# Kernel optimization log

Hardware: AMD Instinct MI355X
Metric: run time of the kernel (lower is better)

## Reference

```python
import jax, jax.numpy as jnp
import numpy as np
import math

B, S, D, H = 8, 256, 4096, 16
HD = D // H  # 256 == S, so the module's transposed mask application is exactly elementwise


def setup_inputs() -> dict:
    key = jax.random.key(0)
    ks = jax.random.split(key, 12)
    sc = 1.0 / math.sqrt(D)
    inp = {
        "q": jax.random.normal(ks[0], (B, S, D), dtype=jnp.float32),
        "k": jax.random.normal(ks[1], (B, S, D), dtype=jnp.float32),
        "v": jax.random.normal(ks[2], (B, S, D), dtype=jnp.float32),
        "mask": jax.random.randint(ks[3], (B, S), 0, 2),
        "Wq": jax.random.normal(ks[4], (D, D), dtype=jnp.float32) * sc,
        "bq": jnp.zeros((D,), dtype=jnp.float32),
        "Wk": jax.random.normal(ks[5], (D, D), dtype=jnp.float32) * sc,
        "bk": jnp.zeros((D,), dtype=jnp.float32),
        "Wv": jax.random.normal(ks[6], (D, D), dtype=jnp.float32) * sc,
        "bv": jnp.zeros((D,), dtype=jnp.float32),
        "Wo": jax.random.normal(ks[7], (D, D), dtype=jnp.float32) * sc,
        "bo": jnp.zeros((D,), dtype=jnp.float32),
    }
    return inp


def reference(q, k, v, mask, Wq, bq, Wk, bk, Wv, bv, Wo, bo):
    def proj(x, W, b):
        # nn.Linear: x @ W.T + b ; then [B,S,H,HD] -> [B,H,S,HD]
        return (x @ W.T + b).reshape(B, S, H, HD).transpose(0, 2, 1, 3)

    qh = proj(q, Wq, bq)
    kh = proj(k, Wk, bk)
    vh = proj(v, Wv, bv)

    # torch: attn_mask = (mask==0).view(bs,1,1,-1).repeat(1,H,HD,1) -> [B,H,HD,S]
    # then where(attn_mask, 0, q) against q of shape [B,H,S,HD] (elementwise since HD==S)
    am = jnp.broadcast_to((mask == 0)[:, None, None, :], (B, H, HD, S))
    qh = jnp.where(am, 0.0, qh)
    kh = jnp.where(am, 0.0, kh)

    scale = 1.0 / math.sqrt(HD)
    scores = jnp.einsum('bhqd,bhkd->bhqk', qh, kh) * scale
    w = jax.nn.softmax(scores, axis=-1)
    out = jnp.einsum('bhqk,bhkd->bhqd', w, vh)
    out = out.transpose(0, 2, 1, 3).reshape(B, S, D)
    out = out * (D ** -0.5)
    return out @ Wo.T + bo
```

## Files before the change

### kernel.cpp

```cpp
#include <hip/hip_runtime.h>


typedef _Float16 f16;
typedef f16 f16x8 __attribute__((ext_vector_type(8)));
typedef float f32x4 __attribute__((ext_vector_type(4)));

__device__ __forceinline__ void g2lds(const f16* g, f16* l) {
  __builtin_amdgcn_global_load_lds((const __attribute__((address_space(1))) void*)g,
                                   (__attribute__((address_space(3))) void*)l, 16, 0, 0);
}

__device__ __forceinline__ void cvt8(const float* src, f16* dst, int i) {
  float4 a = *(const float4*)(src + i);
  float4 b = *(const float4*)(src + i + 4);
  f16x8 o;
  o[0] = (f16)a.x; o[1] = (f16)a.y; o[2] = (f16)a.z; o[3] = (f16)a.w;
  o[4] = (f16)b.x; o[5] = (f16)b.y; o[6] = (f16)b.z; o[7] = (f16)b.w;
  *(f16x8*)(dst + i) = o;
}

__global__ __launch_bounds__(256) void cvt_x(const float* __restrict__ q,
                                             const float* __restrict__ k,
                                             const float* __restrict__ v,
                                             f16* __restrict__ oq, f16* __restrict__ ok,
                                             f16* __restrict__ ov) {
  const float* src; f16* dst;
  if (blockIdx.y == 0)      { src = q; dst = oq; }
  else if (blockIdx.y == 1) { src = k; dst = ok; }
  else                      { src = v; dst = ov; }
  cvt8(src, dst, (blockIdx.x * 256 + threadIdx.x) * 8);
}

__global__ __launch_bounds__(256) void cvt_w2(const float* __restrict__ a,
                                              const float* __restrict__ b,
                                              f16* __restrict__ oa, f16* __restrict__ ob) {
  const float* src; f16* dst;
  if (blockIdx.y == 0) { src = a; dst = oa; }
  else                 { src = b; dst = ob; }
  cvt8(src, dst, (blockIdx.x * 256 + threadIdx.x) * 8);
}

#define MFMA8x(ACC, FA, FB, MO, NO)                                             \
  do {                                                                          \
    __builtin_amdgcn_s_setprio(1);                                              \
    _Pragma("unroll")                                                           \
    for (int m_ = 0; m_ < (MO); ++m_)                                           \
      _Pragma("unroll")                                                         \
      for (int n_ = 0; n_ < (NO); ++n_)                                         \
        _Pragma("unroll")                                                       \
        for (int ks_ = 0; ks_ < 2; ++ks_)                                       \
          ACC = __builtin_amdgcn_mfma_f32_16x16x32_f16(FA[m_][ks_], FB[n_][ks_],\
                                                       ACC, 0, 0, 0);           \
    __builtin_amdgcn_s_setprio(0);                                              \
  } while (0)

__global__ __launch_bounds__(512, 2) void gemm256(
    const f16* __restrict__ Aq, const f16* __restrict__ Ak,
    const float* __restrict__ Bq, const float* __restrict__ Bk,
    const float* __restrict__ bq, const float* __restrict__ bk,
    const int* __restrict__ mask,
    f16* __restrict__ Qbh, f16* __restrict__ Kbh)
{
  __shared__ __align__(16) f16 lds[2][4][8192];
  const int tid = threadIdx.x;
  const int lane = tid & 63, wid = tid >> 6;
  const int wm = wid >> 2, wn = wid & 3;
  const int ln = lane & 15, lh = lane >> 4;
  const int lnx = ln & 7;
  const int K = 4096, NT = 64;

  const int seg = blockIdx.x >> 7;
  int inner = blockIdx.x & 127;
  inner = (inner & 7) * 16 + (inner >> 3);

  const f16* A     = (seg == 0) ? Aq : Ak;
  const float* B   = (seg == 0) ? Bq : Bk;
  const float* bias = (seg == 0) ? bq : bk;
  const int bm = inner % 8, bn = inner / 8;

  const size_t Abase = (size_t)bm * 256 * K;
  const size_t Bbase = (size_t)bn * 256 * K;

  const int sr = tid >> 3;
  const int ss = (tid & 7) ^ (sr & 7);
  const int br = tid >> 2;
  const int bj = tid & 3;
  const int bs0 = ((bj * 2) ^ (br & 7)) * 8;
  const int bs1 = ((bj * 2 + 1) ^ (br & 7)) * 8;

#define STAGE_A(tt, bb_)                                                         \
  do {                                                                           \
    const int kt_ = (tt) << 6;                                                   \
    g2lds(A + Abase + (size_t)sr * K + kt_ + ss * 8,        &lds[bb_][0][0] + tid * 8); \
    g2lds(A + Abase + (size_t)(64 + sr) * K + kt_ + ss * 8, &lds[bb_][0][0] + (512 + tid) * 8); \
    g2lds(A + Abase + (size_t)(128 + sr) * K + kt_ + ss * 8, &lds[bb_][1][0] + tid * 8); \
    g2lds(A + Abase + (size_t)(192 + sr) * K + kt_ + ss * 8, &lds[bb_][1][0] + (512 + tid) * 8); \
  } while (0)

  float4 rb0, rb1, rb2, rb3, rb4, rb5, rb6, rb7;

#define BLOAD(tt)                                                                \
  do {                                                                           \
    const int kt_ = (tt) << 6;                                                   \
    const float* p0_ = B + Bbase + (size_t)br * K + kt_ + bj * 16;               \
    const float* p1_ = B + Bbase + (size_t)(128 + br) * K + kt_ + bj * 16;       \
    rb0 = *(const float4*)(p0_);      rb1 = *(const float4*)(p0_ + 4);           \
    rb2 = *(const float4*)(p0_ + 8);  rb3 = *(const float4*)(p0_ + 12);          \
    rb4 = *(const float4*)(p1_);      rb5 = *(const float4*)(p1_ + 4);           \
    rb6 = *(const float4*)(p1_ + 8);  rb7 = *(const float4*)(p1_ + 12);          \
  } while (0)

#define PACK8(w_, xa_, xb_)                                                      \
  do {                                                                           \
    w_[0] = (f16)xa_.x; w_[1] = (f16)xa_.y; w_[2] = (f16)xa_.z; w_[3] = (f16)xa_.w; \
    w_[4] = (f16)xb_.x; w_[5] = (f16)xb_.y; w_[6] = (f16)xb_.z; w_[7] = (f16)xb_.w; \
  } while (0)

#define BWRITE(bb_)                                                              \
  do {                                                                           \
    f16x8 w0_, w1_, w2_, w3_;                                                    \
    PACK8(w0_, rb0, rb1); PACK8(w1_, rb2, rb3);                                  \
    PACK8(w2_, rb4, rb5); PACK8(w3_, rb6, rb7);                                  \
    *(f16x8*)(&lds[bb_][2][0] + br * 64 + bs0) = w0_;                            \
    *(f16x8*)(&lds[bb_][2][0] + br * 64 + bs1) = w1_;                            \
    *(f16x8*)(&lds[bb_][3][0] + br * 64 + bs0) = w2_;                            \
    *(f16x8*)(&lds[bb_][3][0] + br * 64 + bs1) = w3_;                            \
  } while (0)

#define RD_A03(buf) do { _Pragma("unroll")                                       \
  for (int m_ = 0; m_ < 4; ++m_) _Pragma("unroll")                               \
    for (int k_ = 0; k_ < 2; ++k_)                                               \
      a03[m_][k_] = *(const f16x8*)&(buf)[(m_ * 16 + ln) * 64 + ((k_ * 4 + lh) ^ lnx) * 8]; } while (0)
#define RD_A47(buf) do { _Pragma("unroll")                                       \
  for (int m_ = 0; m_ < 4; ++m_) _Pragma("unroll")                               \
    for (int k_ = 0; k_ < 2; ++k_)                                               \
      a47[m_][k_] = *(const f16x8*)&(buf)[((64 + m_ * 16) + ln) * 64 + ((k_ * 4 + lh) ^ lnx) * 8]; } while (0)
#define RD_B01(buf) do { _Pragma("unroll")                                       \
  for (int n_ = 0; n_ < 2; ++n_) _Pragma("unroll")                               \
    for (int k_ = 0; k_ < 2; ++k_)                                               \
      b01[n_][k_] = *(const f16x8*)&(buf)[(brow + n_ * 16 + ln) * 64 + ((k_ * 4 + lh) ^ lnx) * 8]; } while (0)
#define RD_B23(buf) do { _Pragma("unroll")                                       \
  for (int n_ = 0; n_ < 2; ++n_) _Pragma("unroll")                               \
    for (int k_ = 0; k_ < 2; ++k_)                                               \
      b23[n_][k_] = *(const f16x8*)&(buf)[(brow + 32 + n_ * 16 + ln) * 64 + ((k_ * 4 + lh) ^ lnx) * 8]; } while (0)

  f32x4 acc[8][4] = {};
  f16x8 a03[4][2], a47[4][2], b01[2][2], b23[2][2];
  const int brow = (wn & 1) * 64;

  STAGE_A(0, 0); BLOAD(0);
  asm volatile("s_waitcnt vmcnt(0)" ::: "memory");
  BWRITE(0);
  asm volatile("s_waitcnt lgkmcnt(0)" ::: "memory");
  __builtin_amdgcn_s_barrier();
  {
    const f16* cA0 = &lds[0][wm][0];
    const f16* cB0 = &lds[0][2 + (wn >> 1)][0];
    RD_A03(cA0); RD_B01(cB0);
  }

  for (int t = 0; t < NT; ++t) {
    const int bb = t & 1;
    const f16* cA = &lds[bb][wm][0];
    const f16* cAn = &lds[bb ^ 1][wm][0];
    const f16* cB = &lds[bb][2 + (wn >> 1)][0];
    const f16* cBn = &lds[bb ^ 1][2 + (wn >> 1)][0];

    if (t + 1 < NT) { STAGE_A(t + 1, bb ^ 1); BLOAD(t + 1); }
    RD_B23(cB);
    __builtin_amdgcn_s_barrier();
    MFMA8x(acc[m_][n_], a03, b01, 4, 2);

    RD_A47(cA);
    __builtin_amdgcn_s_barrier();
    MFMA8x(acc[m_][2 + n_], a03, b23, 4, 2);

    __builtin_amdgcn_s_barrier();
    MFMA8x(acc[4 + m_][n_], a47, b01, 4, 2);

    if (t + 1 < NT) {
      asm volatile("s_waitcnt vmcnt(0)" ::: "memory");
      BWRITE(bb ^ 1);
    }
    asm volatile("s_waitcnt lgkmcnt(0)" ::: "memory");
    __builtin_amdgcn_s_barrier();
    if (t + 1 < NT) { RD_A03(cAn); RD_B01(cBn); }
    MFMA8x(acc[4 + m_][2 + n_], a47, b23, 4, 2);
  }
#undef STAGE_A
#undef BLOAD
#undef PACK8
#undef BWRITE
#undef RD_A03
#undef RD_A47
#undef RD_B01
#undef RD_B23

#pragma unroll
  for (int mf = 0; mf < 8; ++mf)
#pragma unroll
    for (int nf = 0; nf < 4; ++nf)
#pragma unroll
      for (int i = 0; i < 4; ++i) {
        int R = bm * 256 + wm * 128 + mf * 16 + lh * 4 + i;
        int C = bn * 256 + wn * 64 + nf * 16 + ln;
        float v = acc[mf][nf][i];
        v += bias[C];
        v = mask[(R >> 8) * 256 + (C & 255)] ? v : 0.0f;
        f16* o = (seg == 0) ? Qbh : Kbh;
        o[(size_t)((R >> 8) * 16 + (C >> 8)) * 65536 +
          (size_t)(R & 255) * 256 + (C & 255)] = (f16)v;
      }
}

template<int EPI>
__global__ __launch_bounds__(512, 2) void gemm_dp(
    const f16* __restrict__ A, const f16* __restrict__ B,
    const float* __restrict__ bias, void* __restrict__ out,
    int M, int N, int K)
{
  __shared__ __align__(16) f16 lds[3 * 24576];
  const int tid = threadIdx.x;
  const int lane = tid & 63, wid = tid >> 6;
  const int wm = wid >> 2, wn = wid & 3;
  const int ln = lane & 15, lh = lane >> 4;
  const int bm = blockIdx.y, bn = blockIdx.x;

  const size_t Abase = (size_t)bm * 128 * K;
  const size_t Bbase = (size_t)bn * 256 * K;
  const int sr = tid >> 3;
  const int ss = (tid & 7) ^ (sr & 7);
  const int NT = K >> 6;

  f16* p0 = &lds[0];
  f16* p1 = &lds[24576];
  f16* p2 = &lds[2 * 24576];

#define STAGE(t_, bo_, part)                                                    \
  do {                                                                          \
    const int kt_ = (t_) << 6;                                                  \
    if ((part) == 0) {                                                          \
      g2lds(A + Abase + (size_t)sr * K + kt_ + ss * 8,         (bo_) + tid * 8);  \
      g2lds(B + Bbase + (size_t)sr * K + kt_ + ss * 8,         (bo_) + 8192 + tid * 8); \
      g2lds(B + Bbase + (size_t)(64 + sr) * K + kt_ + ss * 8,  (bo_) + 8192 + (512 + tid) * 8); \
    } else {                                                                    \
      g2lds(A + Abase + (size_t)(64 + sr) * K + kt_ + ss * 8,  (bo_) + (512 + tid) * 8); \
      g2lds(B + Bbase + (size_t)(128 + sr) * K + kt_ + ss * 8, (bo_) + 8192 + (1024 + tid) * 8); \
      g2lds(B + Bbase + (size_t)(192 + sr) * K + kt_ + ss * 8, (bo_) + 8192 + (1536 + tid) * 8); \
    }                                                                           \
  } while (0)

  const int lx = ln & 7;
  const int arow = (wm * 64 + ln) * 64;
  const int brow = (wn * 64 + ln) * 64;

#define LOADFRAGS(fa, fb, buf, ks)                                              \
  do {                                                                          \
    const f16* bA_ = (buf);                                                     \
    const f16* bB_ = (buf) + 8192;                                              \
    const int so_ = (((ks) * 4 + lh) ^ lx) * 8;                                 \
    _Pragma("unroll")                                                           \
    for (int mf = 0; mf < 4; ++mf)                                              \
      fa[mf] = *(const f16x8*)&bA_[arow + mf * 1024 + so_];                     \
    _Pragma("unroll")                                                           \
    for (int nf = 0; nf < 4; ++nf)                                              \
      fb[nf] = *(const f16x8*)&bB_[brow + nf * 1024 + so_];                     \
  } while (0)

#define MFMA16(fa, fb)                                                          \
  do {                                                                          \
    __builtin_amdgcn_s_setprio(1);                                              \
    _Pragma("unroll")                                                           \
    for (int mf = 0; mf < 4; ++mf)                                              \
      _Pragma("unroll")                                                         \
      for (int nf = 0; nf < 4; ++nf)                                            \
        acc[mf][nf] = __builtin_amdgcn_mfma_f32_16x16x32_f16(fa[mf], fb[nf],    \
                                                             acc[mf][nf], 0, 0, 0); \
    __builtin_amdgcn_s_setprio(0);                                              \
  } while (0)

  f32x4 acc[4][4] = {};
  f16x8 ca[4], cb[4], na[4], nb[4];

  STAGE(0, p0, 0); STAGE(0, p0, 1);
  STAGE(1, p1, 0); STAGE(1, p1, 1);
  asm volatile("s_waitcnt vmcnt(6)" ::: "memory");
  __builtin_amdgcn_s_barrier();
  asm volatile("" ::: "memory");
  LOADFRAGS(ca, cb, p0, 0);

  for (int t = 0; t < NT; ++t) {
    LOADFRAGS(na, nb, p0, 1);
    if (t + 2 < NT) { STAGE(t + 2, p2, 0); STAGE(t + 2, p2, 1); }
    MFMA16(ca, cb);

    if (t + 1 < NT) {
      if (t + 2 < NT) {
        asm volatile("s_waitcnt vmcnt(6)" ::: "memory");
      } else {
        asm volatile("s_waitcnt vmcnt(0)" ::: "memory");
      }
      __builtin_amdgcn_s_barrier();
      asm volatile("" ::: "memory");
      LOADFRAGS(ca, cb, p1, 0);
      MFMA16(na, nb);
      asm volatile("" ::: "memory");
      __builtin_amdgcn_s_barrier();
      asm volatile("" ::: "memory");
      f16* tp = p0; p0 = p1; p1 = p2; p2 = tp;
    } else {
      MFMA16(na, nb);
    }
  }
#undef STAGE
#undef LOADFRAGS
#undef MFMA16

#pragma unroll
  for (int mf = 0; mf < 4; ++mf)
#pragma unroll
    for (int nf = 0; nf < 4; ++nf)
#pragma unroll
      for (int i = 0; i < 4; ++i) {
        int R = bm * 128 + wm * 64 + mf * 16 + lh * 4 + i;
        int C = bn * 256 + wn * 64 + nf * 16 + ln;
        float v = acc[mf][nf][i];
        if (EPI == 1) {
          v += bias[R];
          ((f16*)out)[(size_t)(C >> 8) * 1048576 + (size_t)R * 256 + (C & 255)] = (f16)v;
        } else {
          v += bias[C];
          ((float*)out)[(size_t)R * N + C] = v;
        }
      }
}

__global__ __launch_bounds__(256) void attn_kernel(
    const f16* __restrict__ Q, const f16* __restrict__ Kt,
    const f16* __restrict__ Vt, f16* __restrict__ aout)
{
  __shared__ __align__(16) f16 tile[64 * 256];
  __shared__ __align__(16) f16 pbuf[64 * 256];
  const int tid = threadIdx.x;
  const int lane = tid & 63, w = tid >> 6;
  const int ln = lane & 15, lh = lane >> 4;
  const int bh = blockIdx.x >> 2, rb = blockIdx.x & 3;
  const int b = bh >> 4, h = bh & 15;
  const size_t hb = (size_t)bh * 65536;

  const int strow = tid >> 5;
  const int stsl  = (tid & 31) ^ (strow & 7);

  f16x8 aq[8];
  {
    const f16* qp = Q + hb + (size_t)(rb * 64 + w * 16 + ln) * 256;
#pragma unroll
    for (int ks = 0; ks < 8; ++ks)
      aq[ks] = *(const f16x8*)(qp + ks * 32 + lh * 8);
  }

  f32x4 sacc[16] = {};

  for (int kt = 0; kt < 4; ++kt) {
#pragma unroll
    for (int c = 0; c < 8; ++c) {
      int L = c * 256 + tid;
      int row = c * 8 + strow;
      g2lds(Kt + hb + (size_t)(kt * 64 + row) * 256 + stsl * 8, &tile[L * 8]);
    }
    __syncthreads();
#pragma unroll
    for (int nf = 0; nf < 4; ++nf) {
      f16x8 bf[8];
#pragma unroll
      for (int ks = 0; ks < 8; ++ks) {
        int r = nf * 16 + ln;
        int sl = (ks * 4 + lh) ^ (r & 7);
        bf[ks] = *(const f16x8*)&tile[r * 256 + sl * 8];
      }
#pragma unroll
      for (int ks = 0; ks < 8; ++ks)
        sacc[kt * 4 + nf] = __builtin_amdgcn_mfma_f32_16x16x32_f16(
            aq[ks], bf[ks], sacc[kt * 4 + nf], 0, 0, 0);
    }
    __syncthreads();
  }

  const float SC = 1.0f / 16.0f;
  float mrow[4] = {-1e30f, -1e30f, -1e30f, -1e30f};
#pragma unroll
  for (int t = 0; t < 16; ++t)
#pragma unroll
    for (int i = 0; i < 4; ++i) mrow[i] = fmaxf(mrow[i], sacc[t][i]);
#pragma unroll
  for (int i = 0; i < 4; ++i) {
    mrow[i] = fmaxf(mrow[i], __shfl_xor(mrow[i], 1));
    mrow[i] = fmaxf(mrow[i], __shfl_xor(mrow[i], 2));
    mrow[i] = fmaxf(mrow[i], __shfl_xor(mrow[i], 4));
    mrow[i] = fmaxf(mrow[i], __shfl_xor(mrow[i], 8));
  }
  float ssum[4] = {0.f, 0.f, 0.f, 0.f};
#pragma unroll
  for (int t = 0; t < 16; ++t)
#pragma unroll
    for (int i = 0; i < 4; ++i) {
      float p = __expf((sacc[t][i] - mrow[i]) * SC);
      sacc[t][i] = p;
      ssum[i] += p;
    }
#pragma unroll
  for (int i = 0; i < 4; ++i) {
    ssum[i] += __shfl_xor(ssum[i], 1);
    ssum[i] += __shfl_xor(ssum[i], 2);
    ssum[i] += __shfl_xor(ssum[i], 4);
    ssum[i] += __shfl_xor(ssum[i], 8);
  }
  float rs[4];
#pragma unroll
  for (int i = 0; i < 4; ++i) rs[i] = 1.0f / ssum[i];

#pragma unroll
  for (int t = 0; t < 16; ++t)
#pragma unroll
    for (int i = 0; i < 4; ++i) {
      int row = w * 16 + lh * 4 + i;
      int col = (t >> 2) * 64 + (t & 3) * 16 + ln;
      pbuf[row * 256 + (col ^ ((row & 7) << 3))] = (f16)(sacc[t][i] * rs[i]);
    }

  f16x8 pa[8];
  {
    int r = w * 16 + ln;
#pragma unroll
    for (int ks = 0; ks < 8; ++ks) {
      int col = ks * 32 + lh * 8;
      pa[ks] = *(const f16x8*)&pbuf[r * 256 + (col ^ ((r & 7) << 3))];
    }
  }

  for (int dt = 0; dt < 4; ++dt) {
#pragma unroll
    for (int c = 0; c < 8; ++c) {
      int L = c * 256 + tid;
      int row = c * 8 + strow;
      g2lds(Vt + hb + (size_t)(dt * 64 + row) * 256 + stsl * 8, &tile[L * 8]);
    }
    __syncthreads();
    f32x4 oacc[4] = {};
#pragma unroll
    for (int nf = 0; nf < 4; ++nf) {
      f16x8 bf[8];
#pragma unroll
      for (int ks = 0; ks < 8; ++ks) {
        int r = nf * 16 + ln;
        int sl = (ks * 4 + lh) ^ (r & 7);
        bf[ks] = *(const f16x8*)&tile[r * 256 + sl * 8];
      }
#pragma unroll
      for (int ks = 0; ks < 8; ++ks)
        oacc[nf] = __builtin_amdgcn_mfma_f32_16x16x32_f16(pa[ks], bf[ks], oacc[nf], 0, 0, 0);
    }
#pragma unroll
    for (int nf = 0; nf < 4; ++nf)
#pragma unroll
      for (int i = 0; i < 4; ++i) {
        int s = rb * 64 + w * 16 + lh * 4 + i;
        int d = dt * 64 + nf * 16 + ln;
        aout[(size_t)(b * 256 + s) * 4096 + h * 256 + d] = (f16)(oacc[nf][i] * 0.015625f);
      }
    __syncthreads();
  }
}

extern "C" void kernel_launch(void* const* d_in, const int* in_sizes, int n_in,
                              void* d_out, int out_size, void* d_ws, size_t ws_size,
                              hipStream_t stream) {
  const float* q  = (const float*)d_in[0];
  const float* k  = (const float*)d_in[1];
  const float* v  = (const float*)d_in[2];
  const int*   mk = (const int*)d_in[3];
  const float* Wq = (const float*)d_in[4];
  const float* bq = (const float*)d_in[5];
  const float* Wk = (const float*)d_in[6];
  const float* bk = (const float*)d_in[7];
  const float* Wv = (const float*)d_in[8];
  const float* bv = (const float*)d_in[9];
  const float* Wo = (const float*)d_in[10];
  const float* bo = (const float*)d_in[11];
  float* out = (float*)d_out;

  const size_t NQ = 2048ull * 4096;
  const size_t NW = 4096ull * 4096;
  f16* ws = (f16*)d_ws;
  f16* q16  = ws;
  f16* k16  = q16 + NQ;
  f16* v16  = k16 + NQ;
  f16* Wq16 = v16 + NQ;
  f16* Wk16 = Wq16 + NW;
  f16* Wv16 = Wk16 + NW;
  f16* Wo16 = Wv16 + NW;
  f16* Qbh  = Wo16 + NW;
  f16* Kbh  = Qbh + NQ;
  f16* Vt   = Kbh + NQ;
  f16* at16 = Vt + NQ;

  cvt_x<<<dim3(4096, 3), 256, 0, stream>>>(q, k, v, q16, k16, v16);
  cvt_w2<<<dim3(8192, 2), 256, 0, stream>>>(Wv, Wo, Wv16, Wo16);

  gemm256<<<256, 512, 0, stream>>>(q16, k16, Wq, Wk, bq, bk, mk, Qbh, Kbh);
  gemm_dp<1><<<dim3(8, 32), 512, 0, stream>>>(Wv16, v16, bv, Vt, 4096, 2048, 4096);
  attn_kernel<<<512, 256, 0, stream>>>(Qbh, Kbh, Vt, at16);
  gemm_dp<2><<<dim3(16, 16), 512, 0, stream>>>(at16, Wo16, bo, out, 2048, 4096, 4096);
}
```

Baseline: 419.5 us.

## Pre-convert Wq/Wk to fp16 and stream all QK-GEMM tiles via direct LDS loads

Wq and Wk are now converted to fp16 in the same weight-conversion kernel as Wv and Wo. The Q/K projection GEMM then reads B tiles with global_load_lds directly into LDS, instead of loading fp32 into registers, converting, and writing to LDS. The prefetch schedule is also restructured: the first A chunk of stage t+2 is issued early, and a partial vmcnt wait replaces the full drain. This removes VALU conversion, register pressure and half the B bytes from the GEMM main loop. In exchange it adds an extra pass over 128MB of fp32 weights plus fp16 writes in the conversion kernel.

```diff
diff --git a/kernel.cpp b/kernel.cpp
--- a/kernel.cpp
+++ b/kernel.cpp
@@ -31,12 +31,17 @@
   cvt8(src, dst, (blockIdx.x * 256 + threadIdx.x) * 8);
 }
 
-__global__ __launch_bounds__(256) void cvt_w2(const float* __restrict__ a,
-                                              const float* __restrict__ b,
-                                              f16* __restrict__ oa, f16* __restrict__ ob) {
+__global__ __launch_bounds__(256) void cvt_w(const float* __restrict__ a,
+                                             const float* __restrict__ b,
+                                             const float* __restrict__ c,
+                                             const float* __restrict__ d,
+                                             f16* __restrict__ oa, f16* __restrict__ ob,
+                                             f16* __restrict__ oc, f16* __restrict__ od) {
   const float* src; f16* dst;
-  if (blockIdx.y == 0) { src = a; dst = oa; }
-  else                 { src = b; dst = ob; }
+  if (blockIdx.y == 0)      { src = a; dst = oa; }
+  else if (blockIdx.y == 1) { src = b; dst = ob; }
+  else if (blockIdx.y == 2) { src = c; dst = oc; }
+  else                      { src = d; dst = od; }
   cvt8(src, dst, (blockIdx.x * 256 + threadIdx.x) * 8);
 }
 
@@ -56,7 +61,7 @@
 
 __global__ __launch_bounds__(512, 2) void gemm256(
     const f16* __restrict__ Aq, const f16* __restrict__ Ak,
-    const float* __restrict__ Bq, const float* __restrict__ Bk,
+    const f16* __restrict__ Bq, const f16* __restrict__ Bk,
     const float* __restrict__ bq, const float* __restrict__ bk,
     const int* __restrict__ mask,
     f16* __restrict__ Qbh, f16* __restrict__ Kbh)
@@ -73,58 +78,24 @@
   int inner = blockIdx.x & 127;
   inner = (inner & 7) * 16 + (inner >> 3);
 
-  const f16* A     = (seg == 0) ? Aq : Ak;
-  const float* B   = (seg == 0) ? Bq : Bk;
+  const f16* A   = (seg == 0) ? Aq : Ak;
+  const f16* B   = (seg == 0) ? Bq : Bk;
   const float* bias = (seg == 0) ? bq : bk;
   const int bm = inner % 8, bn = inner / 8;
 
   const size_t Abase = (size_t)bm * 256 * K;
   const size_t Bbase = (size_t)bn * 256 * K;
-
   const int sr = tid >> 3;
   const int ss = (tid & 7) ^ (sr & 7);
-  const int br = tid >> 2;
-  const int bj = tid & 3;
-  const int bs0 = ((bj * 2) ^ (br & 7)) * 8;
-  const int bs1 = ((bj * 2 + 1) ^ (br & 7)) * 8;
-
-#define STAGE_A(tt, bb_)                                                         \
+
+#define STAGEC(tt, bb_, c)                                                       \
   do {                                                                           \
-    const int kt_ = (tt) << 6;                                                   \
-    g2lds(A + Abase + (size_t)sr * K + kt_ + ss * 8,        &lds[bb_][0][0] + tid * 8); \
-    g2lds(A + Abase + (size_t)(64 + sr) * K + kt_ + ss * 8, &lds[bb_][0][0] + (512 + tid) * 8); \
-    g2lds(A + Abase + (size_t)(128 + sr) * K + kt_ + ss * 8, &lds[bb_][1][0] + tid * 8); \
-    g2lds(A + Abase + (size_t)(192 + sr) * K + kt_ + ss * 8, &lds[bb_][1][0] + (512 + tid) * 8); \
-  } while (0)
-
-  float4 rb0, rb1, rb2, rb3, rb4, rb5, rb6, rb7;
-
-#define BLOAD(tt)                                                                \
-  do {                                                                           \
-    const int kt_ = (tt) << 6;                                                   \
-    const float* p0_ = B + Bbase + (size_t)br * K + kt_ + bj * 16;               \
-    const float* p1_ = B + Bbase + (size_t)(128 + br) * K + kt_ + bj * 16;       \
-    rb0 = *(const float4*)(p0_);      rb1 = *(const float4*)(p0_ + 4);           \
-    rb2 = *(const float4*)(p0_ + 8);  rb3 = *(const float4*)(p0_ + 12);          \
-    rb4 = *(const float4*)(p1_);      rb5 = *(const float4*)(p1_ + 4);           \
-    rb6 = *(const float4*)(p1_ + 8);  rb7 = *(const float4*)(p1_ + 12);          \
-  } while (0)
-
-#define PACK8(w_, xa_, xb_)                                                      \
-  do {                                                                           \
-    w_[0] = (f16)xa_.x; w_[1] = (f16)xa_.y; w_[2] = (f16)xa_.z; w_[3] = (f16)xa_.w; \
-    w_[4] = (f16)xb_.x; w_[5] = (f16)xb_.y; w_[6] = (f16)xb_.z; w_[7] = (f16)xb_.w; \
-  } while (0)
-
-#define BWRITE(bb_)                                                              \
-  do {                                                                           \
-    f16x8 w0_, w1_, w2_, w3_;                                                    \
-    PACK8(w0_, rb0, rb1); PACK8(w1_, rb2, rb3);                                  \
-    PACK8(w2_, rb4, rb5); PACK8(w3_, rb6, rb7);                                  \
-    *(f16x8*)(&lds[bb_][2][0] + br * 64 + bs0) = w0_;                            \
-    *(f16x8*)(&lds[bb_][2][0] + br * 64 + bs1) = w1_;                            \
-    *(f16x8*)(&lds[bb_][3][0] + br * 64 + bs0) = w2_;                            \
-    *(f16x8*)(&lds[bb_][3][0] + br * 64 + bs1) = w3_;                            \
+    const f16* base_ = ((c) < 2) ? A + Abase + (size_t)((c) * 128) * K           \
+                                 : B + Bbase + (size_t)(((c) - 2) * 128) * K;    \
+    f16* dst_ = &lds[bb_][c][0];                                                 \
+    g2lds(base_ + (size_t)sr * K + ((tt) << 6) + ss * 8, dst_ + tid * 8);        \
+    g2lds(base_ + (size_t)(64 + sr) * K + ((tt) << 6) + ss * 8,                  \
+          dst_ + (512 + tid) * 8);                                               \
   } while (0)
 
 #define RD_A03(buf) do { _Pragma("unroll")                                       \
@@ -148,10 +119,9 @@
   f16x8 a03[4][2], a47[4][2], b01[2][2], b23[2][2];
   const int brow = (wn & 1) * 64;
 
-  STAGE_A(0, 0); BLOAD(0);
-  asm volatile("s_waitcnt vmcnt(0)" ::: "memory");
-  BWRITE(0);
-  asm volatile("s_waitcnt lgkmcnt(0)" ::: "memory");
+  STAGEC(0, 0, 0); STAGEC(0, 0, 1); STAGEC(0, 0, 2); STAGEC(0, 0, 3);
+  STAGEC(1, 1, 0);
+  asm volatile("s_waitcnt vmcnt(2)" ::: "memory");
   __builtin_amdgcn_s_barrier();
   {
     const f16* cA0 = &lds[0][wm][0];
@@ -162,11 +132,11 @@
   for (int t = 0; t < NT; ++t) {
     const int bb = t & 1;
     const f16* cA = &lds[bb][wm][0];
+    const f16* cB = &lds[bb][2 + (wn >> 1)][0];
     const f16* cAn = &lds[bb ^ 1][wm][0];
-    const f16* cB = &lds[bb][2 + (wn >> 1)][0];
     const f16* cBn = &lds[bb ^ 1][2 + (wn >> 1)][0];
 
-    if (t + 1 < NT) { STAGE_A(t + 1, bb ^ 1); BLOAD(t + 1); }
+    if (t + 1 < NT) { STAGEC(t + 1, bb ^ 1, 1); STAGEC(t + 1, bb ^ 1, 2); STAGEC(t + 1, bb ^ 1, 3); }
     RD_B23(cB);
     __builtin_amdgcn_s_barrier();
     MFMA8x(acc[m_][n_], a03, b01, 4, 2);
@@ -178,19 +148,18 @@
     __builtin_amdgcn_s_barrier();
     MFMA8x(acc[4 + m_][n_], a47, b01, 4, 2);
 
-    if (t + 1 < NT) {
+    if (t + 2 < NT) {
+      STAGEC(t + 2, bb, 0);
+      asm volatile("s_waitcnt vmcnt(2)" ::: "memory");
+    } else {
       asm volatile("s_waitcnt vmcnt(0)" ::: "memory");
-      BWRITE(bb ^ 1);
     }
     asm volatile("s_waitcnt lgkmcnt(0)" ::: "memory");
     __builtin_amdgcn_s_barrier();
     if (t + 1 < NT) { RD_A03(cAn); RD_B01(cBn); }
     MFMA8x(acc[4 + m_][2 + n_], a47, b23, 4, 2);
   }
-#undef STAGE_A
-#undef BLOAD
-#undef PACK8
-#undef BWRITE
+#undef STAGEC
 #undef RD_A03
 #undef RD_A47
 #undef RD_B01
@@ -505,9 +474,9 @@
   f16* at16 = Vt + NQ;
 
   cvt_x<<<dim3(4096, 3), 256, 0, stream>>>(q, k, v, q16, k16, v16);
-  cvt_w2<<<dim3(8192, 2), 256, 0, stream>>>(Wv, Wo, Wv16, Wo16);
-
-  gemm256<<<256, 512, 0, stream>>>(q16, k16, Wq, Wk, bq, bk, mk, Qbh, Kbh);
+  cvt_w<<<dim3(8192, 4), 256, 0, stream>>>(Wq, Wk, Wv, Wo, Wq16, Wk16, Wv16, Wo16);
+
+  gemm256<<<256, 512, 0, stream>>>(q16, k16, Wq16, Wk16, bq, bk, mk, Qbh, Kbh);
   gemm_dp<1><<<dim3(8, 32), 512, 0, stream>>>(Wv16, v16, bv, Vt, 4096, 2048, 4096);
   attn_kernel<<<512, 256, 0, stream>>>(Qbh, Kbh, Vt, at16);
   gemm_dp<2><<<dim3(16, 16), 512, 0, stream>>>(at16, Wo16, bo, out, 2048, 4096, 4096);
```

Result: faster. 368.1 us (-12.2%).
